# Optimization experiments

Measured on AMD Instinct MI355X. Metric: run time of the kernel, lower is better.

## Reference

```python
import jax, jax.numpy as jnp
import numpy as np

NUM_EMBEDDINGS = 1024
EMBEDDING_DIM = 256
COMMITMENT_COST = 0.25
DECAY = 0.99
EPSILON = 1e-5


def setup_inputs() -> dict:
    key = jax.random.key(0)
    k1, k2 = jax.random.split(key)
    B, C, D, H, W = 4, EMBEDDING_DIM, 16, 32, 32
    z = jax.random.normal(k1, (B, C, D, H, W), dtype=jnp.float32)
    bound = 1.0 / (EMBEDDING_DIM ** 0.5)  # nn.init.uniform_(-1/sqrt(d), 1/sqrt(d))
    embed = jax.random.uniform(k2, (NUM_EMBEDDINGS, EMBEDDING_DIM), dtype=jnp.float32,
                               minval=-bound, maxval=bound)
    ema_cluster_size = jnp.zeros((NUM_EMBEDDINGS,), dtype=jnp.float32)
    ema_embed_sum = embed  # buffer initialized as a clone of the embedding weight
    return {"z": z, "embed": embed,
            "ema_cluster_size": ema_cluster_size, "ema_embed_sum": ema_embed_sum}


def reference(z, embed, ema_cluster_size, ema_embed_sum):
    """Training-mode forward of VectorQuantizer (EMA codebook update included).

    Returns (z_q [B,C,D,H,W], vq_loss scalar, indices [B,D,H,W]).
    """
    K, Dm = embed.shape
    B, C, D, H, W = z.shape
    # (B,C,D,H,W) -> (B,D,H,W,C) -> (N, Dm)
    zp = jnp.transpose(z, (0, 2, 3, 4, 1))
    zf = zp.reshape(-1, Dm)

    # squared-distance via expanded cdist: |z|^2 + |e|^2 - 2 z e^T
    dist = (jnp.sum(zf * zf, axis=1, keepdims=True)
            + jnp.sum(embed * embed, axis=1)
            - 2.0 * jnp.matmul(zf, embed.T))  # (N, K)
    idx = jnp.argmin(dist, axis=1)  # (N,)

    # EMA statistics (one-hot matmuls expressed as segment sums)
    batch_cluster_size = jax.ops.segment_sum(jnp.ones_like(idx, dtype=zf.dtype), idx,
                                             num_segments=K)
    batch_embed_sum = jax.ops.segment_sum(zf, idx, num_segments=K)  # (K, Dm)
    new_ema_cs = DECAY * ema_cluster_size + (1.0 - DECAY) * batch_cluster_size
    new_ema_es = DECAY * ema_embed_sum + (1.0 - DECAY) * batch_embed_sum
    n = jnp.sum(new_ema_cs)
    cluster_size = (new_ema_cs + EPSILON) / (n + K * EPSILON) * n
    new_embed = new_ema_es / cluster_size[:, None]  # updated codebook, used for gather

    z_q = new_embed[idx].reshape(zp.shape)  # (B,D,H,W,C)
    vq_loss = COMMITMENT_COST * jnp.mean((zp - jax.lax.stop_gradient(z_q)) ** 2)
    z_q = zp + jax.lax.stop_gradient(z_q - zp)  # straight-through

    indices = idx.reshape(B, D, H, W)
    z_q = jnp.transpose(z_q, (0, 4, 1, 2, 3))  # back to (B,C,D,H,W)
    return z_q, vq_loss, indices
```

## Files before the change

kernel.cpp:

```cpp
#include <hip/hip_runtime.h>
#include <hip/hip_bf16.h>
#include <cfloat>

#define NTOT    65536
#define KCODES  1024
#define DM      256
#define SPAT    16384
#define ZQ_SIZE 16777216

#define WS_ENORM 0
#define WS_CSIZE 1024
#define WS_START 2048
#define WS_LOSSP 3104
#define WS_HIST  11296
#define WS_SORT  273440
#define WS_IDX   338976
#define WS_NEWE  404512

__global__ __launch_bounds__(256) void enorm_kernel(const float* __restrict__ embed,
                                                    float* __restrict__ enorm) {
    int k = blockIdx.x;
    int t = threadIdx.x;
    float v = embed[k * DM + t];
    v *= v;
    #pragma unroll
    for (int m = 32; m > 0; m >>= 1) v += __shfl_xor(v, m);
    __shared__ float sm[4];
    if ((t & 63) == 0) sm[t >> 6] = v;
    __syncthreads();
    if (t == 0) enorm[k] = sm[0] + sm[1] + sm[2] + sm[3];
}

__global__ __launch_bounds__(256, 3) void argmin_kernel(
    const float* __restrict__ z, const float* __restrict__ embed,
    const float* __restrict__ enorm, int* __restrict__ idx_out,
    float* __restrict__ dout, float* __restrict__ zt) {
    __shared__ float zs[64][68];
    __shared__ float es[128][68];

    const int tid = threadIdx.x;
    const int n0  = blockIdx.x * 64;
    const int b   = n0 >> 14;
    const int s0  = n0 & 16383;
    const int ti  = tid >> 4;
    const int tj  = tid & 15;
    const int sl  = tid & 63;
    const int cg  = tid >> 6;
    const int ex  = tid >> 4;
    const int ec  = (tid & 15) * 4;

    float best[4]  = {FLT_MAX, FLT_MAX, FLT_MAX, FLT_MAX};
    int   bestk[4] = {0, 0, 0, 0};
    float acc[4][8];

    float  zr[16];
    float4 er[8];

    {
        const float* zp = z + (size_t)(b * DM + cg * 16) * SPAT + s0 + sl;
        #pragma unroll
        for (int u = 0; u < 16; ++u) zr[u] = zp[(size_t)u * SPAT];
        #pragma unroll
        for (int v = 0; v < 8; ++v)
            er[v] = *(const float4*)&embed[(size_t)(ex + v * 16) * DM + ec];
    }

    for (int it = 0; it < 32; ++it) {
        const int c0 = (it & 3) * 64;
        const int k0 = (it >> 2) * 128;

        __syncthreads();
        #pragma unroll
        for (int u = 0; u < 16; ++u) zs[sl][cg * 16 + u] = zr[u];
        #pragma unroll
        for (int v = 0; v < 8; ++v) *(float4*)&es[ex + v * 16][ec] = er[v];
        __syncthreads();

        if (it + 1 < 32) {
            const int c1 = ((it + 1) & 3) * 64;
            const int k1 = ((it + 1) >> 2) * 128;
            const float* zp = z + (size_t)(b * DM + c1 + cg * 16) * SPAT + s0 + sl;
            #pragma unroll
            for (int u = 0; u < 16; ++u) zr[u] = zp[(size_t)u * SPAT];
            #pragma unroll
            for (int v = 0; v < 8; ++v)
                er[v] = *(const float4*)&embed[(size_t)(k1 + ex + v * 16) * DM + c1 + ec];
        }

        if (it < 4) {
            #pragma unroll
            for (int u = 0; u < 4; ++u) {
                int row = (tid >> 4) + u * 16;
                float4 v4 = *(const float4*)&zs[row][(tid & 15) * 4];
                *(float4*)&zt[(size_t)(n0 + row) * DM + c0 + (tid & 15) * 4] = v4;
            }
        }

        if ((it & 3) == 0) {
            #pragma unroll
            for (int i = 0; i < 4; ++i)
                #pragma unroll
                for (int j = 0; j < 8; ++j) acc[i][j] = 0.f;
        }

        #pragma unroll 4
        for (int c = 0; c < 64; c += 4) {
            float4 za[4], eb[8];
            #pragma unroll
            for (int i = 0; i < 4; ++i) za[i] = *(const float4*)&zs[ti + i * 16][c];
            #pragma unroll
            for (int j = 0; j < 8; ++j) eb[j] = *(const float4*)&es[tj + j * 16][c];
            #pragma unroll
            for (int i = 0; i < 4; ++i)
                #pragma unroll
                for (int j = 0; j < 8; ++j) {
                    acc[i][j] = fmaf(za[i].x, eb[j].x, acc[i][j]);
                    acc[i][j] = fmaf(za[i].y, eb[j].y, acc[i][j]);
                    acc[i][j] = fmaf(za[i].z, eb[j].z, acc[i][j]);
                    acc[i][j] = fmaf(za[i].w, eb[j].w, acc[i][j]);
                }
        }

        if ((it & 3) == 3) {
            #pragma unroll
            for (int j = 0; j < 8; ++j) {
                int q = k0 + tj + j * 16;
                float en = enorm[q];
                #pragma unroll
                for (int i = 0; i < 4; ++i) {
                    float v = fmaf(-2.0f, acc[i][j], en);
                    if (v < best[i]) { best[i] = v; bestk[i] = q; }
                }
            }
        }
    }

    #pragma unroll
    for (int i = 0; i < 4; ++i) {
        float bd = best[i];
        int   bk = bestk[i];
        #pragma unroll
        for (int m = 1; m < 16; m <<= 1) {
            float od = __shfl_xor(bd, m);
            int   ok = __shfl_xor(bk, m);
            if (od < bd || (od == bd && ok < bk)) { bd = od; bk = ok; }
        }
        if (tj == 0) {
            int n = n0 + ti + i * 16;
            idx_out[n] = bk;
            dout[ZQ_SIZE + 1 + n] = (float)bk;
        }
    }
}

__global__ __launch_bounds__(256) void hist_kernel(const int* __restrict__ idx,
                                                   int* __restrict__ hist) {
    __shared__ int lh[KCODES];
    int ch = blockIdx.x, t = threadIdx.x;
    #pragma unroll
    for (int u = 0; u < 4; ++u) lh[t + u * 256] = 0;
    __syncthreads();
    int k = idx[ch * 256 + t];
    atomicAdd(&lh[k], 1);
    __syncthreads();
    #pragma unroll
    for (int u = 0; u < 4; ++u)
        hist[ch * KCODES + t + u * 256] = lh[t + u * 256];
}

__global__ __launch_bounds__(1024) void scan_kernel(
    int* __restrict__ hist, const float* __restrict__ ema_cs,
    int* __restrict__ start, float* __restrict__ csize) {
    int k = threadIdx.x;
    int run = 0;
    for (int ch = 0; ch < 256; ++ch) {
        int t = hist[ch * KCODES + k];
        hist[ch * KCODES + k] = run;
        run += t;
    }
    int lane = k & 63, wv = k >> 6;
    int v = run;
    #pragma unroll
    for (int d = 1; d < 64; d <<= 1) {
        int t = __shfl_up(v, d);
        if (lane >= d) v += t;
    }
    __shared__ int wsum[16];
    if (lane == 63) wsum[wv] = v;
    __syncthreads();
    __shared__ int wpre[16];
    if (k == 0) {
        int s = 0;
        #pragma unroll
        for (int i = 0; i < 16; ++i) { wpre[i] = s; s += wsum[i]; }
    }
    __syncthreads();
    int excl = wpre[wv] + v - run;
    start[k] = excl;
    if (k == 1023) start[1024] = excl + run;
    float ncs = 0.99f * ema_cs[k] + 0.01f * (float)run;
    float r = ncs;
    #pragma unroll
    for (int m = 32; m > 0; m >>= 1) r += __shfl_xor(r, m);
    __shared__ float fs[16];
    if (lane == 0) fs[wv] = r;
    __syncthreads();
    __shared__ float nt;
    if (k == 0) {
        float s = 0.f;
        #pragma unroll
        for (int i = 0; i < 16; ++i) s += fs[i];
        nt = s;
    }
    __syncthreads();
    float n = nt;
    csize[k] = (ncs + 1e-5f) / (n + 1024.0f * 1e-5f) * n;
}

__global__ __launch_bounds__(256) void rank_scatter_kernel(
    const int* __restrict__ idx, const int* __restrict__ hist,
    const int* __restrict__ start, int* __restrict__ sorted) {
    __shared__ int lidx[256];
    int ch = blockIdx.x, t = threadIdx.x;
    int k = idx[ch * 256 + t];
    lidx[t] = k;
    __syncthreads();
    int rank = 0;
    for (int j = 0; j < 255; ++j)
        if (j < t && lidx[j] == k) ++rank;
    sorted[start[k] + hist[ch * KCODES + k] + rank] = ch * 256 + t;
}

__global__ __launch_bounds__(256) void gather_kernel(
    const float* __restrict__ zt, const int* __restrict__ sorted,
    const int* __restrict__ start, const float* __restrict__ ema_es,
    const float* __restrict__ csize, float* __restrict__ newe) {
    int k = blockIdx.x, c = threadIdx.x;
    int s0 = start[k], s1 = start[k + 1];
    float acc = 0.f;
    for (int i = s0; i < s1; ++i) {
        int n = sorted[i];
        acc += zt[(size_t)n * DM + c];
    }
    size_t o = (size_t)k * DM + c;
    newe[o] = (0.99f * ema_es[o] + 0.01f * acc) / csize[k];
}

__global__ __launch_bounds__(256) void output_kernel(
    const float* __restrict__ z, const float* __restrict__ newe,
    const int* __restrict__ idx, float* __restrict__ dout,
    float* __restrict__ lossp) {
    int gid = blockIdx.x * 256 + threadIdx.x;
    float lsum = 0.f;
    #pragma unroll
    for (int it = 0; it < 8; ++it) {
        int o = gid + it * (8192 * 256);
        int s = o & 16383, t2 = o >> 14;
        int c = t2 & 255, b = t2 >> 8;
        int n = (b << 14) + s;
        int k = idx[n];
        float v = newe[(size_t)k * DM + c];
        float zv = z[o];
        dout[o] = v;
        float d = zv - v;
        lsum = fmaf(d, d, lsum);
    }
    #pragma unroll
    for (int m = 32; m > 0; m >>= 1) lsum += __shfl_xor(lsum, m);
    __shared__ float sm[4];
    int t = threadIdx.x;
    if ((t & 63) == 0) sm[t >> 6] = lsum;
    __syncthreads();
    if (t == 0) lossp[blockIdx.x] = sm[0] + sm[1] + sm[2] + sm[3];
}

__global__ __launch_bounds__(256) void loss_final_kernel(const float* __restrict__ lossp,
                                                         float* __restrict__ dout) {
    int t = threadIdx.x;
    float v = 0.f;
    for (int i = t; i < 8192; i += 256) v += lossp[i];
    #pragma unroll
    for (int m = 32; m > 0; m >>= 1) v += __shfl_xor(v, m);
    __shared__ float sm[4];
    if ((t & 63) == 0) sm[t >> 6] = v;
    __syncthreads();
    if (t == 0) dout[ZQ_SIZE] = 0.25f * ((sm[0] + sm[1] + sm[2] + sm[3]) / 16777216.0f);
}

extern "C" void kernel_launch(void* const* d_in, const int* in_sizes, int n_in,
                              void* d_out, int out_size, void* d_ws, size_t ws_size,
                              hipStream_t stream) {
    const float* z      = (const float*)d_in[0];
    const float* embed  = (const float*)d_in[1];
    const float* ema_cs = (const float*)d_in[2];
    const float* ema_es = (const float*)d_in[3];
    float* out = (float*)d_out;
    float* ws  = (float*)d_ws;

    float* enorm = ws + WS_ENORM;
    float* csize = ws + WS_CSIZE;
    int*   start = (int*)(ws + WS_START);
    float* lossp = ws + WS_LOSSP;
    int*   hist  = (int*)(ws + WS_HIST);
    int*   sortd = (int*)(ws + WS_SORT);
    int*   idx   = (int*)(ws + WS_IDX);
    float* newe  = ws + WS_NEWE;
    float* zt    = out;

    enorm_kernel<<<KCODES, 256, 0, stream>>>(embed, enorm);
    argmin_kernel<<<NTOT / 64, 256, 0, stream>>>(z, embed, enorm, idx, out, zt);
    hist_kernel<<<256, 256, 0, stream>>>(idx, hist);
    scan_kernel<<<1, 1024, 0, stream>>>(hist, ema_cs, start, csize);
    rank_scatter_kernel<<<256, 256, 0, stream>>>(idx, hist, start, sortd);
    gather_kernel<<<KCODES, 256, 0, stream>>>(zt, sortd, start, ema_es, csize, newe);
    output_kernel<<<8192, 256, 0, stream>>>(z, newe, idx, out, lossp);
    loss_final_kernel<<<1, 256, 0, stream>>>(lossp, out);
}
```

Before: 732.2 us.

## Double-buffer argmin tiles with direct global-to-LDS loads and swizzled layout

Rewrites the distance/argmin kernel's staging so z and codebook tiles go straight from global memory into a double-buffered LDS area, instead of passing through registers. The channel chunk shrinks from 64 to 16 and the codebook tile gets an XOR swizzle to avoid bank conflicts. The inner product loop is reorganised as outer products over 4 contiguous z rows, and the occupancy hint rises to 4 blocks per CU. The aim is to overlap loading with FMA work and to cut register pressure. The cost is four times as many block barriers, and correctness depends on async LDS writes being complete at each barrier.

```diff
diff --git a/kernel.cpp b/kernel.cpp
--- a/kernel.cpp
+++ b/kernel.cpp
@@ -17,6 +17,10 @@
 #define WS_IDX   338976
 #define WS_NEWE  404512
 
+#define GLOAD_LDS16(gp, lp) __builtin_amdgcn_global_load_lds( \
+    (const __attribute__((address_space(1))) unsigned int*)(gp), \
+    (__attribute__((address_space(3))) unsigned int*)(lp), 16, 0, 0)
+
 __global__ __launch_bounds__(256) void enorm_kernel(const float* __restrict__ embed,
                                                     float* __restrict__ enorm) {
     int k = blockIdx.x;
@@ -31,12 +35,12 @@
     if (t == 0) enorm[k] = sm[0] + sm[1] + sm[2] + sm[3];
 }
 
-__global__ __launch_bounds__(256, 3) void argmin_kernel(
+__global__ __launch_bounds__(256, 4) void argmin_kernel(
     const float* __restrict__ z, const float* __restrict__ embed,
     const float* __restrict__ enorm, int* __restrict__ idx_out,
     float* __restrict__ dout, float* __restrict__ zt) {
-    __shared__ float zs[64][68];
-    __shared__ float es[128][68];
+    __shared__ __align__(16) float zs[2][16][64];
+    __shared__ __align__(16) float es[2][128][16];
 
     const int tid = threadIdx.x;
     const int n0  = blockIdx.x * 64;
@@ -44,84 +48,86 @@
     const int s0  = n0 & 16383;
     const int ti  = tid >> 4;
     const int tj  = tid & 15;
-    const int sl  = tid & 63;
-    const int cg  = tid >> 6;
-    const int ex  = tid >> 4;
-    const int ec  = (tid & 15) * 4;
-
-    float best[4]  = {FLT_MAX, FLT_MAX, FLT_MAX, FLT_MAX};
-    int   bestk[4] = {0, 0, 0, 0};
-    float acc[4][8];
-
-    float  zr[16];
-    float4 er[8];
-
-    {
-        const float* zp = z + (size_t)(b * DM + cg * 16) * SPAT + s0 + sl;
-        #pragma unroll
-        for (int u = 0; u < 16; ++u) zr[u] = zp[(size_t)u * SPAT];
-        #pragma unroll
-        for (int v = 0; v < 8; ++v)
-            er[v] = *(const float4*)&embed[(size_t)(ex + v * 16) * DM + ec];
-    }
-
-    for (int it = 0; it < 32; ++it) {
-        const int c0 = (it & 3) * 64;
-        const int k0 = (it >> 2) * 128;
+    const int w   = tid >> 6;
+    const int l   = tid & 63;
+
+    auto stage_z = [&](int st, int buf) {
+        const int c0 = (st & 15) * 16;
+        int cc = c0 + w * 4 + (l >> 4);
+        const float* gp = z + (size_t)(b * DM + cc) * SPAT + s0 + (l & 15) * 4;
+        GLOAD_LDS16(gp, &zs[buf][w * 4][0]);
+    };
+    auto stage_es = [&](int st, int buf) {
+        const int k0 = (st >> 4) * 128;
+        const int c0 = (st & 15) * 16;
+        #pragma unroll
+        for (int v = 0; v < 2; ++v) {
+            int R = w * 32 + v * 16;
+            int r = R + (l >> 2);
+            int sg = (l & 3) ^ ((l >> 2) & 3);
+            const float* gp = embed + (size_t)(k0 + r) * DM + c0 + sg * 4;
+            GLOAD_LDS16(gp, &es[buf][R][0]);
+        }
+    };
+
+    stage_z(0, 0);
+    stage_es(0, 0);
+
+    float best[4], acc[4][8];
+    int   bestk[4];
+    #pragma unroll
+    for (int i = 0; i < 4; ++i) { best[i] = FLT_MAX; bestk[i] = 0; }
+
+    #pragma unroll 1
+    for (int st = 0; st < 128; ++st) {
+        const int buf = st & 1;
+        const int k0  = (st >> 4) * 128;
 
         __syncthreads();
-        #pragma unroll
-        for (int u = 0; u < 16; ++u) zs[sl][cg * 16 + u] = zr[u];
-        #pragma unroll
-        for (int v = 0; v < 8; ++v) *(float4*)&es[ex + v * 16][ec] = er[v];
-        __syncthreads();
-
-        if (it + 1 < 32) {
-            const int c1 = ((it + 1) & 3) * 64;
-            const int k1 = ((it + 1) >> 2) * 128;
-            const float* zp = z + (size_t)(b * DM + c1 + cg * 16) * SPAT + s0 + sl;
-            #pragma unroll
-            for (int u = 0; u < 16; ++u) zr[u] = zp[(size_t)u * SPAT];
-            #pragma unroll
-            for (int v = 0; v < 8; ++v)
-                er[v] = *(const float4*)&embed[(size_t)(k1 + ex + v * 16) * DM + c1 + ec];
-        }
-
-        if (it < 4) {
-            #pragma unroll
-            for (int u = 0; u < 4; ++u) {
-                int row = (tid >> 4) + u * 16;
-                float4 v4 = *(const float4*)&zs[row][(tid & 15) * 4];
-                *(float4*)&zt[(size_t)(n0 + row) * DM + c0 + (tid & 15) * 4] = v4;
-            }
-        }
-
-        if ((it & 3) == 0) {
+
+        if (st < 127) { stage_z(st + 1, buf ^ 1); stage_es(st + 1, buf ^ 1); }
+
+        if (st < 16) {
+            const int c0 = st * 16;
+            int r = tid >> 2, cg = tid & 3;
+            float4 v4;
+            v4.x = zs[buf][cg * 4 + 0][r];
+            v4.y = zs[buf][cg * 4 + 1][r];
+            v4.z = zs[buf][cg * 4 + 2][r];
+            v4.w = zs[buf][cg * 4 + 3][r];
+            *(float4*)&zt[(size_t)(n0 + r) * DM + c0 + cg * 4] = v4;
+        }
+
+        if ((st & 15) == 0) {
             #pragma unroll
             for (int i = 0; i < 4; ++i)
                 #pragma unroll
                 for (int j = 0; j < 8; ++j) acc[i][j] = 0.f;
         }
 
-        #pragma unroll 4
-        for (int c = 0; c < 64; c += 4) {
-            float4 za[4], eb[8];
+        #pragma unroll
+        for (int cq = 0; cq < 4; ++cq) {
+            float4 zq[4];
             #pragma unroll
-            for (int i = 0; i < 4; ++i) za[i] = *(const float4*)&zs[ti + i * 16][c];
+            for (int q = 0; q < 4; ++q)
+                zq[q] = *(const float4*)&zs[buf][cq * 4 + q][ti * 4];
+            const int eoff = ((cq ^ (tj & 3)) << 2);
             #pragma unroll
-            for (int j = 0; j < 8; ++j) eb[j] = *(const float4*)&es[tj + j * 16][c];
-            #pragma unroll
-            for (int i = 0; i < 4; ++i)
+            for (int j = 0; j < 8; ++j) {
+                float4 eb = *(const float4*)&es[buf][tj + j * 16][eoff];
                 #pragma unroll
-                for (int j = 0; j < 8; ++j) {
-                    acc[i][j] = fmaf(za[i].x, eb[j].x, acc[i][j]);
-                    acc[i][j] = fmaf(za[i].y, eb[j].y, acc[i][j]);
-                    acc[i][j] = fmaf(za[i].z, eb[j].z, acc[i][j]);
-                    acc[i][j] = fmaf(za[i].w, eb[j].w, acc[i][j]);
+                for (int q = 0; q < 4; ++q) {
+                    float ec = (q == 0) ? eb.x : (q == 1) ? eb.y
+                             : (q == 2) ? eb.z : eb.w;
+                    acc[0][j] = fmaf(zq[q].x, ec, acc[0][j]);
+                    acc[1][j] = fmaf(zq[q].y, ec, acc[1][j]);
+                    acc[2][j] = fmaf(zq[q].z, ec, acc[2][j]);
+                    acc[3][j] = fmaf(zq[q].w, ec, acc[3][j]);
                 }
-        }
-
-        if ((it & 3) == 3) {
+            }
+        }
+
+        if ((st & 15) == 15) {
             #pragma unroll
             for (int j = 0; j < 8; ++j) {
                 int q = k0 + tj + j * 16;
@@ -146,7 +152,7 @@
             if (od < bd || (od == bd && ok < bk)) { bd = od; bk = ok; }
         }
         if (tj == 0) {
-            int n = n0 + ti + i * 16;
+            int n = n0 + ti * 4 + i;
             idx_out[n] = bk;
             dout[ZQ_SIZE + 1 + n] = (float)bk;
         }
```

After: 750.8 us. 1.03x slower.
